# Kernel tuning notes

Hardware: AMD Instinct MI355X
Metric: run time of the kernel (lower is better)

The kernel has to match this reference:

```python
import jax, jax.numpy as jnp
import numpy as np

# FSUSqrt config: mode='unipolar', emit=True, entry_sr=2
# nsadd = FSUAdd(mode='unipolar', scale=1, dima=0, depth=10): offset=0,
# accumulator clamped to +/- 2**(depth-2) = 256, emits 1 when acc >= scale.
ACC_MIN = -256.0
ACC_MAX = 256.0
SCALE = 1.0
T, N = 64, 524288
ENTRY_SR = 2


def setup_inputs() -> dict:
    key = jax.random.key(0)
    # bit-stream input: T clock cycles of N parallel bits in {0,1}
    x = jax.random.randint(key, (T, N), 0, 2).astype(jnp.float32)
    emit_init = jnp.zeros((N,), dtype=jnp.float32)          # self.emit_out
    acc_init = jnp.zeros((N,), dtype=jnp.float32)           # nsadd accumulator
    # ShiftReg init: sr[i] = i % 2, broadcast over elements -> [ENTRY_SR, N]
    sr_init = jnp.broadcast_to(
        (jnp.arange(ENTRY_SR) % 2).astype(jnp.float32)[:, None], (ENTRY_SR, N)
    )
    return {"input": x, "emit_init": emit_init, "acc_init": acc_init, "sr_init": sr_init}


def reference(input, emit_init, acc_init, sr_init):
    """Runs T sequential calls of FSUSqrt.forward (emit=True, unipolar) via lax.scan.
    All bit values are 0/1 floats; bitwise AND == multiply on {0,1}."""

    def step(carry, x_t):
        emit, acc, sr = carry
        # in_stack = stack([input, emit_out]); FSUAdd sums over dim 0, offset=0
        acc = jnp.clip(acc + x_t + emit, ACC_MIN, ACC_MAX)
        out = (acc >= SCALE).astype(jnp.float32)
        acc = acc - out * SCALE
        # unipolar_emit: invert output, scramble through shift register, AND
        out_inv = 1.0 - out
        scrambled = sr[0]  # self.idx is never updated -> index 0 always
        sr = jnp.concatenate([out_inv[None, :], sr[:-1]], axis=0)
        emit = scrambled * out  # AND of {0,1} bits
        return (emit, acc, sr), out

    _, outs = jax.lax.scan(step, (emit_init, acc_init, sr_init), input)
    return outs  # [T, N] bit-stream, stype=float
```

## Files before the change

### kernel.cpp

```cpp
#include <hip/hip_runtime.h>


constexpr int T = 64;
constexpr int N = 524288;
constexpr int NV = N / 4;
constexpr int BLOCK = 256;

__device__ __forceinline__ float stepf(float x, float& acc, float& emit, float& sr0) {
    float a = acc + x + emit;
    a = fminf(fmaxf(a, -256.0f), 256.0f);
    float o = (a >= 1.0f) ? 1.0f : 0.0f;
    acc = a - o;
    float e = sr0 * o;
    sr0 = 1.0f - o;
    emit = e;
    return o;
}

__global__ __launch_bounds__(BLOCK) void fsusqrt_kernel(
    const float4* __restrict__ x,
    const float4* __restrict__ emit_init,
    const float4* __restrict__ acc_init,
    const float4* __restrict__ sr_init,
    float4* __restrict__ out)
{
    const int i = blockIdx.x * BLOCK + threadIdx.x;
    if (i >= NV) return;

    float4 emit = emit_init[i];
    float4 acc  = acc_init[i];
    float4 sr0  = sr_init[i];

    float4 buf0 = x[i];
    float4 buf1 = x[NV + i];

    #pragma unroll
    for (int t = 0; t < T; ++t) {
        float4 cur = buf0;
        buf0 = buf1;
        if (t + 2 < T) buf1 = x[(t + 2) * NV + i];

        float4 o;
        o.x = stepf(cur.x, acc.x, emit.x, sr0.x);
        o.y = stepf(cur.y, acc.y, emit.y, sr0.y);
        o.z = stepf(cur.z, acc.z, emit.z, sr0.z);
        o.w = stepf(cur.w, acc.w, emit.w, sr0.w);

        out[t * NV + i] = o;
    }
}

extern "C" void kernel_launch(void* const* d_in, const int* in_sizes, int n_in,
                              void* d_out, int out_size, void* d_ws, size_t ws_size,
                              hipStream_t stream) {
    const float4* x         = (const float4*)d_in[0];
    const float4* emit_init = (const float4*)d_in[1];
    const float4* acc_init  = (const float4*)d_in[2];
    const float4* sr_init   = (const float4*)d_in[3];
    float4* out = (float4*)d_out;

    dim3 grid(NV / BLOCK);
    dim3 block(BLOCK);
    fsusqrt_kernel<<<grid, block, 0, stream>>>(x, emit_init, acc_init, sr_init, out);
}
```

Measured before the change: 47.32 us.

## Use float2 per thread, deeper prefetch, and nontemporal loads/stores

Each thread now handles two elements instead of four, which doubles the grid to 1024 blocks and raises parallelism across the CUs. The prefetch depth for the streamed input grows from two to four timesteps. Input loads and output stores are marked nontemporal to avoid cache pollution on this purely streaming workload. The trade-off is narrower 8-byte memory transactions instead of 16-byte ones.

```diff
diff --git a/kernel.cpp b/kernel.cpp
--- a/kernel.cpp
+++ b/kernel.cpp
@@ -3,8 +3,11 @@
 
 constexpr int T = 64;
 constexpr int N = 524288;
-constexpr int NV = N / 4;
+constexpr int NV2 = N / 2;
 constexpr int BLOCK = 256;
+constexpr int PF = 4;
+
+typedef float f32x2 __attribute__((ext_vector_type(2)));
 
 __device__ __forceinline__ float stepf(float x, float& acc, float& emit, float& sr0) {
     float a = acc + x + emit;
@@ -18,48 +21,51 @@
 }
 
 __global__ __launch_bounds__(BLOCK) void fsusqrt_kernel(
-    const float4* __restrict__ x,
-    const float4* __restrict__ emit_init,
-    const float4* __restrict__ acc_init,
-    const float4* __restrict__ sr_init,
-    float4* __restrict__ out)
+    const f32x2* __restrict__ x,
+    const f32x2* __restrict__ emit_init,
+    const f32x2* __restrict__ acc_init,
+    const f32x2* __restrict__ sr_init,
+    f32x2* __restrict__ out)
 {
     const int i = blockIdx.x * BLOCK + threadIdx.x;
-    if (i >= NV) return;
 
-    float4 emit = emit_init[i];
-    float4 acc  = acc_init[i];
-    float4 sr0  = sr_init[i];
+    const f32x2 ev = emit_init[i];
+    const f32x2 av = acc_init[i];
+    const f32x2 sv = sr_init[i];
 
-    float4 buf0 = x[i];
-    float4 buf1 = x[NV + i];
+    float emitx = ev.x, emity = ev.y;
+    float accx  = av.x, accy  = av.y;
+    float sr0x  = sv.x, sr0y  = sv.y;
+
+    f32x2 buf[PF];
+    #pragma unroll
+    for (int t = 0; t < PF; ++t)
+        buf[t] = __builtin_nontemporal_load(&x[t * NV2 + i]);
 
     #pragma unroll
     for (int t = 0; t < T; ++t) {
-        float4 cur = buf0;
-        buf0 = buf1;
-        if (t + 2 < T) buf1 = x[(t + 2) * NV + i];
+        f32x2 cur = buf[t % PF];
+        if (t + PF < T)
+            buf[t % PF] = __builtin_nontemporal_load(&x[(t + PF) * NV2 + i]);
 
-        float4 o;
-        o.x = stepf(cur.x, acc.x, emit.x, sr0.x);
-        o.y = stepf(cur.y, acc.y, emit.y, sr0.y);
-        o.z = stepf(cur.z, acc.z, emit.z, sr0.z);
-        o.w = stepf(cur.w, acc.w, emit.w, sr0.w);
+        f32x2 o;
+        o.x = stepf(cur.x, accx, emitx, sr0x);
+        o.y = stepf(cur.y, accy, emity, sr0y);
 
-        out[t * NV + i] = o;
+        __builtin_nontemporal_store(o, &out[t * NV2 + i]);
     }
 }
 
 extern "C" void kernel_launch(void* const* d_in, const int* in_sizes, int n_in,
                               void* d_out, int out_size, void* d_ws, size_t ws_size,
                               hipStream_t stream) {
-    const float4* x         = (const float4*)d_in[0];
-    const float4* emit_init = (const float4*)d_in[1];
-    const float4* acc_init  = (const float4*)d_in[2];
-    const float4* sr_init   = (const float4*)d_in[3];
-    float4* out = (float4*)d_out;
+    const f32x2* x         = (const f32x2*)d_in[0];
+    const f32x2* emit_init = (const f32x2*)d_in[1];
+    const f32x2* acc_init  = (const f32x2*)d_in[2];
+    const f32x2* sr_init   = (const f32x2*)d_in[3];
+    f32x2* out = (f32x2*)d_out;
 
-    dim3 grid(NV / BLOCK);
+    dim3 grid(NV2 / BLOCK);
     dim3 block(BLOCK);
     fsusqrt_kernel<<<grid, block, 0, stream>>>(x, emit_init, acc_init, sr_init, out);
 }
```

After: 49.06 us. +3.7%, slower.
